# Kernel tuning notes

Measured on AMD Instinct MI355X. Metric: run time of the kernel, lower is better.

The kernel has to match this reference:

```python
import jax, jax.numpy as jnp
import numpy as np

B, N, H, N_NODE = 512, 256, 128, 50000
ALPHA, BETA, DEGREE = 0.8, 0.1, 2


def setup_inputs() -> dict:
    key = jax.random.key(0)
    k1, k2, k3 = jax.random.split(key, 3)
    inputs = jax.random.randint(k1, (B, N), 0, N_NODE, dtype=jnp.int64)
    A = jax.random.uniform(k2, (B, N, 2 * N), dtype=jnp.float32)
    emb_weight = jax.random.normal(k3, (N_NODE, H), dtype=jnp.float32)
    return {"inputs": inputs, "A": A, "emb_weight": emb_weight}


def reference(inputs, A, emb_weight):
    # embedding lookup: [B, N, H]
    hidden = emb_weight[inputs]
    n = A.shape[1]
    # merge in/out adjacency halves
    A2 = A[:, :, :n] + A[:, :, n:2 * n]
    I = jnp.eye(n, dtype=A2.dtype)
    adj = A2 + I  # add self-loops
    # symmetric renormalization D^-1/2 (A+I) D^-1/2, vectorized over batch
    row_sum = adj.sum(axis=-1)  # [B, N]
    d_inv_sqrt = jnp.power(row_sum, -0.5)
    d_inv_sqrt = jnp.where(jnp.isinf(d_inv_sqrt), 0.0, d_inv_sqrt)
    norm_adj = adj * d_inv_sqrt[:, :, None] * d_inv_sqrt[:, None, :]
    # sgc_embed == 1 mixing: alpha * norm + beta * (1 - norm) * I
    A_mix = ALPHA * norm_adj + BETA * (1.0 - norm_adj) * I
    # SGC propagation: degree rounds of batched matmul
    for _ in range(DEGREE):
        hidden = jnp.einsum('bij,bjd->bid', A_mix, hidden)
    return hidden
```

## Files before the change

kernel.cpp:

```cpp
#include <hip/hip_runtime.h>

typedef __attribute__((ext_vector_type(8))) __bf16 bf16x8;
typedef __attribute__((ext_vector_type(4))) float f32x4;
typedef __attribute__((ext_vector_type(8))) unsigned short u16x8;
typedef __attribute__((ext_vector_type(4))) unsigned short u16x4;

#define B_SZ 512

static __device__ __forceinline__ float bf2f(unsigned short u) {
    unsigned int x = ((unsigned int)u) << 16;
    return __builtin_bit_cast(float, x);
}
static __device__ __forceinline__ unsigned short f2bf(float f) {
    unsigned int x = __builtin_bit_cast(unsigned int, f);
    x += 0x7FFFu + ((x >> 16) & 1u);
    return (unsigned short)(x >> 16);
}

__global__ __launch_bounds__(256) void detect_kernel(const int4* __restrict__ idx4,
                                                     int* __restrict__ flag) {
    int t = blockIdx.x * 256 + threadIdx.x;
    int any = 0;
#pragma unroll
    for (int r = 0; r < 2; r++) {
        int4 v = idx4[t + r * 16384];
        any |= (v.y | v.w);
    }
    if (any) atomicOr(flag, 1);
}

__global__ __launch_bounds__(512) void fused_kernel(const int* __restrict__ idx,
                                                    const float* __restrict__ A,
                                                    const float* __restrict__ emb,
                                                    const int* __restrict__ flag,
                                                    float* __restrict__ outF) {
    __shared__ __align__(16) unsigned char smem[132096];
    float* dL = (float*)(smem + 131072);

    int b = blockIdx.x;
    int tid = threadIdx.x;
    int w = tid >> 6;
    int lane = tid & 63;
    int q = lane >> 4;
    int ln = lane & 15;

    const float* Ab = A + (size_t)b * 256 * 512;

    for (int rr = 0; rr < 32; rr += 4) {
        f32x4 va[4], vb[4];
#pragma unroll
        for (int u = 0; u < 4; u++) {
            const float* p = Ab + (size_t)(w * 32 + rr + u) * 512 + lane * 4;
            va[u] = *(const f32x4*)p;
            vb[u] = *(const f32x4*)(p + 256);
        }
#pragma unroll
        for (int u = 0; u < 4; u++) {
            int row = w * 32 + rr + u;
            f32x4 a2 = va[u] + vb[u];
            u16x4 pk;
#pragma unroll
            for (int e = 0; e < 4; e++) pk[e] = f2bf(a2[e]);
            int byte_ = ((row << 9) + (lane << 3)) ^ ((row & 7) << 4);
            *(u16x4*)(smem + byte_) = pk;
            float s = a2[0] + a2[1] + a2[2] + a2[3];
#pragma unroll
            for (int m = 32; m >= 1; m >>= 1) s += __shfl_xor(s, m, 64);
            if (lane == 0) dL[row] = 1.0f / sqrtf(s + 1.0f);
        }
    }
    __syncthreads();

    int j = tid & 255;
    int hh = tid >> 8;
    int pos = b * 256 + j;
    int node = (flag[0] != 0) ? idx[pos] : idx[2 * pos];
    const float* erow = emb + (size_t)node * 128 + hh * 64;
    f32x4 ev[16];
#pragma unroll
    for (int p = 0; p < 16; p++) ev[p] = *(const f32x4*)(erow + p * 4);

    bf16x8 afr[2][8];
#pragma unroll
    for (int s = 0; s < 8; s++) {
        f32x4 dc0 = *(const f32x4*)(dL + s * 32 + q * 8);
        f32x4 dc1 = *(const f32x4*)(dL + s * 32 + q * 8 + 4);
#pragma unroll
        for (int mt = 0; mt < 2; mt++) {
            int r = w * 32 + mt * 16 + ln;
            int byte_ = ((r << 9) + s * 64 + q * 16) ^ ((r & 7) << 4);
            u16x8 a = *(const u16x8*)(smem + byte_);
            float dr = dL[r];
            u16x8 o;
#pragma unroll
            for (int e = 0; e < 8; e++) {
                int c = s * 32 + q * 8 + e;
                float av = bf2f(a[e]);
                bool diag = (r == c);
                if (diag) av += 1.0f;
                float na = av * dr * ((e < 4) ? dc0[e] : dc1[e - 4]);
                float v = 0.8f * na;
                if (diag) v += 0.1f * (1.0f - na);
                o[e] = f2bf(v);
            }
            afr[mt][s] = __builtin_bit_cast(bf16x8, o);
        }
    }
    __syncthreads();

#pragma unroll
    for (int p = 0; p < 16; p++) {
#pragma unroll
        for (int e = 0; e < 4; e++) {
            int h = hh * 64 + p * 4 + e;
            int byte_ = ((h << 9) + (j << 1)) ^ ((h & 7) << 4);
            *(unsigned short*)(smem + byte_) = f2bf(ev[p][e]);
        }
    }
    __syncthreads();

    f32x4 acc[2][8];
#pragma unroll
    for (int mt = 0; mt < 2; mt++)
#pragma unroll
        for (int nt = 0; nt < 8; nt++) acc[mt][nt] = f32x4{0.f, 0.f, 0.f, 0.f};

#pragma unroll
    for (int s = 0; s < 8; s++) {
        bf16x8 bfr[8];
#pragma unroll
        for (int nt = 0; nt < 8; nt++) {
            int h = nt * 16 + ln;
            int byte_ = ((h << 9) + s * 64 + q * 16) ^ ((h & 7) << 4);
            bfr[nt] = *(const bf16x8*)(smem + byte_);
        }
#pragma unroll
        for (int mt = 0; mt < 2; mt++)
#pragma unroll
            for (int nt = 0; nt < 8; nt++)
                acc[mt][nt] = __builtin_amdgcn_mfma_f32_16x16x32_bf16(
                    afr[mt][s], bfr[nt], acc[mt][nt], 0, 0, 0);
    }

#pragma unroll
    for (int mt = 0; mt < 2; mt++)
#pragma unroll
        for (int nt = 0; nt < 8; nt++) {
            int h = nt * 16 + ln;
            int i0 = w * 32 + mt * 16 + q * 4;
            u16x4 pk;
#pragma unroll
            for (int r = 0; r < 4; r++) pk[r] = f2bf(acc[mt][nt][r]);
            int byte_ = 65536 + (((h << 9) + (i0 << 1)) ^ ((h & 7) << 4));
            *(u16x4*)(smem + byte_) = pk;
            acc[mt][nt] = f32x4{0.f, 0.f, 0.f, 0.f};
        }
    __syncthreads();

#pragma unroll
    for (int s = 0; s < 8; s++) {
        bf16x8 bfr[8];
#pragma unroll
        for (int nt = 0; nt < 8; nt++) {
            int h = nt * 16 + ln;
            int byte_ = 65536 + (((h << 9) + s * 64 + q * 16) ^ ((h & 7) << 4));
            bfr[nt] = *(const bf16x8*)(smem + byte_);
        }
#pragma unroll
        for (int mt = 0; mt < 2; mt++)
#pragma unroll
            for (int nt = 0; nt < 8; nt++)
                acc[mt][nt] = __builtin_amdgcn_mfma_f32_16x16x32_bf16(
                    afr[mt][s], bfr[nt], acc[mt][nt], 0, 0, 0);
    }

#pragma unroll
    for (int mt = 0; mt < 2; mt++)
#pragma unroll
        for (int nt = 0; nt < 8; nt++) {
            int h = nt * 16 + ln;
            int i0 = w * 32 + mt * 16 + q * 4;
#pragma unroll
            for (int r = 0; r < 4; r++)
                outF[((size_t)b * 256 + i0 + r) * 128 + h] = acc[mt][nt][r];
        }
}

extern "C" void kernel_launch(void* const* d_in, const int* in_sizes, int n_in,
                              void* d_out, int out_size, void* d_ws, size_t ws_size,
                              hipStream_t stream) {
    const int* idx = (const int*)d_in[0];
    const float* A = (const float*)d_in[1];
    const float* emb = (const float*)d_in[2];
    float* out = (float*)d_out;

    int* flag = (int*)d_ws;

    hipMemsetAsync(flag, 0, 4, stream);
    detect_kernel<<<64, 256, 0, stream>>>((const int4*)idx, flag);
    fused_kernel<<<B_SZ, 512, 0, stream>>>(idx, A, emb, flag, out);
}
```

Baseline: 440.7 us.

## Split adjacency merge and row-sum into a separate kernel to shrink LDS

Moves the A-half merge, bf16 packing and degree computation into a standalone rowsum kernel that writes a bf16 merged adjacency and d^-1/2 to workspace. The main kernel then reads A fragments straight from global memory and reuses one 64KB LDS buffer for both propagation rounds. This lowers per-block LDS from about 129KB to about 65KB so more blocks can be resident per CU. The cost is an extra global round trip for the bf16 adjacency (about 64MB written and read) plus one more kernel launch.

```diff
diff --git a/kernel.cpp b/kernel.cpp
--- a/kernel.cpp
+++ b/kernel.cpp
@@ -29,13 +29,33 @@
     if (any) atomicOr(flag, 1);
 }
 
-__global__ __launch_bounds__(512) void fused_kernel(const int* __restrict__ idx,
-                                                    const float* __restrict__ A,
-                                                    const float* __restrict__ emb,
-                                                    const int* __restrict__ flag,
-                                                    float* __restrict__ outF) {
-    __shared__ __align__(16) unsigned char smem[132096];
-    float* dL = (float*)(smem + 131072);
+__global__ __launch_bounds__(256) void rowsum_kernel(const float* __restrict__ A,
+                                                     unsigned short* __restrict__ a2,
+                                                     float* __restrict__ d) {
+    int row = blockIdx.x * 4 + (threadIdx.x >> 6);
+    int lane = threadIdx.x & 63;
+    const float* p = A + (size_t)row * 512 + lane * 4;
+    f32x4 vin = *(const f32x4*)p;
+    f32x4 vout = *(const f32x4*)(p + 256);
+    f32x4 v = vin + vout;
+    float s = v[0] + v[1] + v[2] + v[3];
+    u16x4 pk;
+#pragma unroll
+    for (int e = 0; e < 4; e++) pk[e] = f2bf(v[e]);
+    *(u16x4*)(a2 + (size_t)row * 256 + lane * 4) = pk;
+#pragma unroll
+    for (int m = 32; m >= 1; m >>= 1) s += __shfl_xor(s, m, 64);
+    if (lane == 0) d[row] = 1.0f / sqrtf(s + 1.0f);
+}
+
+__global__ __launch_bounds__(512, 4) void main_kernel(const int* __restrict__ idx,
+                                                      const unsigned short* __restrict__ a2,
+                                                      const float* __restrict__ dG,
+                                                      const float* __restrict__ emb,
+                                                      const int* __restrict__ flag,
+                                                      float* __restrict__ outF) {
+    __shared__ __align__(16) unsigned char smem[66560];
+    float* dL = (float*)(smem + 65536);
 
     int b = blockIdx.x;
     int tid = threadIdx.x;
@@ -44,32 +64,7 @@
     int q = lane >> 4;
     int ln = lane & 15;
 
-    const float* Ab = A + (size_t)b * 256 * 512;
-
-    for (int rr = 0; rr < 32; rr += 4) {
-        f32x4 va[4], vb[4];
-#pragma unroll
-        for (int u = 0; u < 4; u++) {
-            const float* p = Ab + (size_t)(w * 32 + rr + u) * 512 + lane * 4;
-            va[u] = *(const f32x4*)p;
-            vb[u] = *(const f32x4*)(p + 256);
-        }
-#pragma unroll
-        for (int u = 0; u < 4; u++) {
-            int row = w * 32 + rr + u;
-            f32x4 a2 = va[u] + vb[u];
-            u16x4 pk;
-#pragma unroll
-            for (int e = 0; e < 4; e++) pk[e] = f2bf(a2[e]);
-            int byte_ = ((row << 9) + (lane << 3)) ^ ((row & 7) << 4);
-            *(u16x4*)(smem + byte_) = pk;
-            float s = a2[0] + a2[1] + a2[2] + a2[3];
-#pragma unroll
-            for (int m = 32; m >= 1; m >>= 1) s += __shfl_xor(s, m, 64);
-            if (lane == 0) dL[row] = 1.0f / sqrtf(s + 1.0f);
-        }
-    }
-    __syncthreads();
+    if (tid < 256) dL[tid] = dG[b * 256 + tid];
 
     int j = tid & 255;
     int hh = tid >> 8;
@@ -80,6 +75,9 @@
 #pragma unroll
     for (int p = 0; p < 16; p++) ev[p] = *(const f32x4*)(erow + p * 4);
 
+    __syncthreads();
+
+    const unsigned short* Ab = a2 + (size_t)b * 256 * 256;
     bf16x8 afr[2][8];
 #pragma unroll
     for (int s = 0; s < 8; s++) {
@@ -88,8 +86,7 @@
 #pragma unroll
         for (int mt = 0; mt < 2; mt++) {
             int r = w * 32 + mt * 16 + ln;
-            int byte_ = ((r << 9) + s * 64 + q * 16) ^ ((r & 7) << 4);
-            u16x8 a = *(const u16x8*)(smem + byte_);
+            u16x8 a = *(const u16x8*)(Ab + r * 256 + s * 32 + q * 8);
             float dr = dL[r];
             u16x8 o;
 #pragma unroll
@@ -106,7 +103,6 @@
             afr[mt][s] = __builtin_bit_cast(bf16x8, o);
         }
     }
-    __syncthreads();
 
 #pragma unroll
     for (int p = 0; p < 16; p++) {
@@ -141,6 +137,7 @@
                 acc[mt][nt] = __builtin_amdgcn_mfma_f32_16x16x32_bf16(
                     afr[mt][s], bfr[nt], acc[mt][nt], 0, 0, 0);
     }
+    __syncthreads();
 
 #pragma unroll
     for (int mt = 0; mt < 2; mt++)
@@ -151,7 +148,7 @@
             u16x4 pk;
 #pragma unroll
             for (int r = 0; r < 4; r++) pk[r] = f2bf(acc[mt][nt][r]);
-            int byte_ = 65536 + (((h << 9) + (i0 << 1)) ^ ((h & 7) << 4));
+            int byte_ = ((h << 9) + (i0 << 1)) ^ ((h & 7) << 4);
             *(u16x4*)(smem + byte_) = pk;
             acc[mt][nt] = f32x4{0.f, 0.f, 0.f, 0.f};
         }
@@ -163,7 +160,7 @@
 #pragma unroll
         for (int nt = 0; nt < 8; nt++) {
             int h = nt * 16 + ln;
-            int byte_ = 65536 + (((h << 9) + s * 64 + q * 16) ^ ((h & 7) << 4));
+            int byte_ = ((h << 9) + s * 64 + q * 16) ^ ((h & 7) << 4);
             bfr[nt] = *(const bf16x8*)(smem + byte_);
         }
 #pragma unroll
@@ -194,9 +191,13 @@
     const float* emb = (const float*)d_in[2];
     float* out = (float*)d_out;
 
-    int* flag = (int*)d_ws;
+    char* ws = (char*)d_ws;
+    int* flag = (int*)ws;
+    float* d = (float*)(ws + 4096);
+    unsigned short* a2 = (unsigned short*)(ws + 528384);
 
     hipMemsetAsync(flag, 0, 4, stream);
     detect_kernel<<<64, 256, 0, stream>>>((const int4*)idx, flag);
-    fused_kernel<<<B_SZ, 512, 0, stream>>>(idx, A, emb, flag, out);
-}
+    rowsum_kernel<<<B_SZ * 256 / 4, 256, 0, stream>>>(A, a2, d);
+    main_kernel<<<B_SZ, 512, 0, stream>>>(idx, a2, d, emb, flag, out);
+}
```

After: 589.1 us. 1.34x slower.
